# Performance work log

Measured on AMD Instinct MI355X. Metric: run time of the kernel, lower is better.

Reference implementation:

```python
import jax, jax.numpy as jnp
import numpy as np

B, C, T = 8, 64, 128

def _conv(x, w, b, stride=1, pad=1, groups=1):
    y = jax.lax.conv_general_dilated(x, w, (stride, stride), [(pad, pad), (pad, pad)],
                                     feature_group_count=groups,
                                     dimension_numbers=('NCHW', 'OIHW', 'NCHW'))
    return y + b[None, :, None, None]

def _lrelu(x):
    return jnp.where(x > 0, x, 0.1 * x)

def _ps4(A, Bt, Ct, Dt):
    # qiancha(A,B,C,D) interleaves channels with stride 4; PixelShuffle(2) then maps
    # group index j in [0..3] to pixel offset (j//2, j%2): A->(0,0), B->(0,1), C->(1,0), D->(1,1)
    b, c, h, w = A.shape
    s = jnp.stack([A, Bt, Ct, Dt], axis=2).reshape(b, c, 2, 2, h, w)
    return s.transpose(0, 1, 4, 2, 5, 3).reshape(b, c, 2 * h, 2 * w)

def _il2(A, Bt):
    # qiancha2: stride-2 channel interleave
    b, c, h, w = A.shape
    return jnp.stack([A, Bt], axis=2).reshape(b, 2 * c, h, w)

def setup_inputs():
    key = jax.random.key(0)
    ks = jax.random.split(key, 20)
    def w(k, shape):
        return 0.05 * jax.random.normal(k, shape, dtype=jnp.float32)
    d = {}
    d['x'] = jax.random.normal(ks[0], (B, C, T, T), dtype=jnp.float32)
    d['w_hwc'] = w(ks[1], (3 * C, C, 1, 1)); d['b_hwc'] = w(ks[2], (3 * C,))
    d['w_dw'] = w(ks[3], (3 * C, 1, 3, 3)); d['b_dw'] = w(ks[4], (3 * C,))
    d['w_hw'] = w(ks[5], (C, C, 3, 3)); d['b_hw'] = w(ks[6], (C,))
    d['w_cw'] = w(ks[7], (T, T, 3, 3)); d['b_cw'] = w(ks[8], (T,))
    d['w_hc'] = w(ks[9], (T, T, 3, 3)); d['b_hc'] = w(ks[10], (T,))
    d['w_down'] = w(ks[11], (C, 2 * C, 2, 2)); d['b_down'] = w(ks[12], (C,))
    d['w_l1'] = w(ks[13], (C, C, 3, 3)); d['b_l1'] = w(ks[14], (C,))
    d['w_l2'] = w(ks[15], (C, C, 3, 3)); d['b_l2'] = w(ks[16], (C,))
    return d

def reference(x, w_hwc, b_hwc, w_dw, b_dw, w_hw, b_hw, w_cw, b_cw, w_hc, b_hc,
              w_down, b_down, w_l1, b_l1, w_l2, b_l2):
    c = x.shape[1]
    # 1x1 expand then depthwise 3x3 -> three gating maps
    hwc = _conv(_conv(x, w_hwc, b_hwc, pad=0), w_dw, b_dw, pad=1, groups=3 * c)
    HW, CW, HC = jnp.split(hwc, 3, axis=1)
    x_hw = _lrelu(_conv(x, w_hw, b_hw)) * HW
    x_cw = _lrelu(_conv(x.transpose(0, 2, 1, 3), w_cw, b_cw)).transpose(0, 2, 1, 3) * CW
    x_hc = _lrelu(_conv(x.transpose(0, 3, 2, 1), w_hc, b_hc)).transpose(0, 3, 2, 1) * HC
    xqc1 = _ps4(x, x_hw, x_cw, x_hc)
    xqc2 = _ps4(x_hc, x_cw, x_hw, x)
    xqc = _il2(xqc1, xqc2)                              # [B, 2C, 2T, 2T]
    out = _conv(xqc, w_down, b_down, stride=2, pad=0) + x
    out1 = _lrelu(_conv(out, w_l1, b_l1))
    out1 = _lrelu(_conv(out1, w_l2, b_l2))
    return x + out1
```

## Files before the change

kernel.cpp:

```cpp
#include <hip/hip_runtime.h>
#include <hip/hip_bf16.h>

#define BB 8
#define CC 64
#define TT 128
#define PP (TT*TT)
#define C3 192

typedef __hip_bfloat16 bf16;
typedef __attribute__((ext_vector_type(8))) short short8;
typedef __attribute__((ext_vector_type(4))) float floatx4;

__device__ __forceinline__ float b2f(bf16 v){ return __bfloat162float(v); }
__device__ __forceinline__ bf16 f2b(float v){ return __float2bfloat16(v); }
__device__ __forceinline__ short8 lds8(const bf16* p){ return *(const short8*)(const void*)p; }

__global__ void k_wpk(const float* __restrict__ w_down, const float* __restrict__ w_hc,
                      const float* __restrict__ w_cw,  const float* __restrict__ w_hwc,
                      const float* __restrict__ w_hw,  const float* __restrict__ w_l1,
                      const float* __restrict__ w_l2,  const float* __restrict__ w_dw,
                      const float* __restrict__ b_hwc, const float* __restrict__ b_dw,
                      bf16* __restrict__ wpkd,
                      bf16* __restrict__ wpkhw, bf16* __restrict__ wpkl1,
                      bf16* __restrict__ wpkl2, bf16* __restrict__ wpkcw,
                      bf16* __restrict__ wpkhc, bf16* __restrict__ wpkg,
                      float* __restrict__ bg){
  int i = blockIdx.x*256 + threadIdx.x;
  if (i < 147456){
    int j = i & 7, lane = (i>>3) & 63, mm = (i>>9) & 7, kk = (i>>12) & 3, t = i >> 14;
    int m = mm*16 + (lane & 15);
    int k = kk*32 + (lane>>4)*8 + j;
    wpkcw[i] = f2b(w_cw[m*1152 + k*9 + t]);
    wpkhc[i] = f2b(w_hc[m*1152 + k*9 + t]);
  }
  if (i < 36864){
    int j = i & 7, lane = (i>>3) & 63, mm = (i>>9) & 3, kk = (i>>11) & 1, t = i >> 12;
    int oc = mm*16 + (lane & 15);
    int ic = kk*32 + (lane>>4)*8 + j;
    int s = oc*576 + ic*9 + t;
    wpkhw[i] = f2b(w_hw[s]);
    wpkl1[i] = f2b(w_l1[s]);
    wpkl2[i] = f2b(w_l2[s]);
  }
  if (i < 110592){
    int j = i & 7, lane = (i>>3) & 63, rest = i >> 9;
    int mm = rest % 12, tk = rest / 12;
    int oc = mm*16 + (lane & 15);
    int ic = (tk & 1)*32 + (lane>>4)*8 + j;
    int t = tk >> 1;
    wpkg[i] = f2b(w_dw[oc*9 + t] * w_hwc[oc*64 + ic]);
  }
  if (i < 1728){
    int cls = i / C3, oc = i % C3;
    int ch = cls / 3, cw = cls % 3;
    float S = 0.f;
    for (int dh = (ch==0?1:0); dh <= (ch==2?1:2); ++dh)
      for (int dw = (cw==0?1:0); dw <= (cw==2?1:2); ++dw)
        S += w_dw[oc*9 + dh*3 + dw];
    bg[cls*C3 + oc] = b_dw[oc] + b_hwc[oc]*S;
  }
  if (i < 16384){
    int j = i & 7, lane = (i>>3) & 63, mm = (i>>9) & 3, kk = i >> 11;
    int m = mm*16 + (lane & 15);
    int k = kk*32 + (lane>>4)*8 + j;
    int s = k >> 6, c = k & 63;
    wpkd[i] = f2b(w_down[m*512 + c*8 + s] + w_down[m*512 + c*8 + 7 - s]);
  }
}

__global__ void k_pack(const float* __restrict__ x, bf16* __restrict__ xh,
                       bf16* __restrict__ xb16){
  int h = blockIdx.x, b = blockIdx.y;
  __shared__ float xs[64][129];
  for (int idx = threadIdx.x; idx < 2048; idx += 256){
    int c = idx >> 5, w4 = (idx & 31)*4;
    float4 v = *(const float4*)(x + ((size_t)b*CC + c)*PP + h*TT + w4);
    bf16 o4[4] = { f2b(v.x), f2b(v.y), f2b(v.z), f2b(v.w) };
    *(uint2*)(xb16 + ((size_t)b*CC + c)*PP + h*TT + w4) = *(uint2*)o4;
    xs[c][w4] = v.x; xs[c][w4+1] = v.y; xs[c][w4+2] = v.z; xs[c][w4+3] = v.w;
  }
  __syncthreads();
  for (int idx = threadIdx.x; idx < 8192; idx += 256){
    int w = idx >> 6, c = idx & 63;
    xh[(((size_t)b*TT + h)*TT + w)*64 + c] = f2b(xs[c][w]);
  }
}

__global__ void k_xw(const float* __restrict__ x, bf16* __restrict__ xW){
  int c = blockIdx.x, b = blockIdx.y;
  __shared__ float xs2[32][129];
  const float* src = x + ((size_t)b*CC + c)*PP;
  bf16* dst = xW + ((size_t)b*CC + c)*PP;
  for (int s = 0; s < 4; ++s){
    for (int idx = threadIdx.x; idx < 4096; idx += 256){
      int hl = idx >> 7, w = idx & 127;
      xs2[hl][w] = src[(s*32 + hl)*TT + w];
    }
    __syncthreads();
    for (int idx = threadIdx.x; idx < 4096; idx += 256){
      int w = idx >> 5, hl = idx & 31;
      dst[w*TT + s*32 + hl] = f2b(xs2[hl][w]);
    }
    __syncthreads();
  }
}

__global__ __launch_bounds__(256)
void k_g3x3m(const bf16* __restrict__ xh, const bf16* __restrict__ wpkg,
             const float* __restrict__ bg, bf16* __restrict__ g){
  int w0b = blockIdx.x*64, h = blockIdx.y, b = blockIdx.z;
  int tid = threadIdx.x, lane = tid & 63, wv = tid >> 6;
  int nlo = lane & 15, quad = lane >> 4;
  __shared__ bf16 xs[3][66][64];
  for (int idx = tid; idx < 1584; idx += 256){
    int dh = idx / 528, r = idx % 528, wi = r >> 3, ch = r & 7;
    int gh = h + dh - 1, gw = w0b + wi - 1;
    uint4 v = make_uint4(0,0,0,0);
    if (gh >= 0 && gh < TT && gw >= 0 && gw < TT)
      v = *(const uint4*)(xh + (((size_t)b*TT + gh)*TT + gw)*64 + ch*8);
    *(uint4*)(&xs[dh][wi][((ch ^ (wi & 7)))*8]) = v;
  }
  __syncthreads();
  floatx4 acc[3][4] = {};
  #pragma unroll
  for (int t = 0; t < 9; ++t){
    int dh = t/3, dw = t%3;
    int swk = (nlo + dw) & 7;
    #pragma unroll
    for (int kk = 0; kk < 2; ++kk){
      int pc = ((kk*4 + quad) ^ swk)*8;
      short8 bfv[4];
      #pragma unroll
      for (int nn = 0; nn < 4; ++nn)
        bfv[nn] = lds8(&xs[dh][nn*16 + nlo + dw][pc]);
      #pragma unroll
      for (int ml = 0; ml < 3; ++ml){
        short8 a = *(const short8*)(const void*)(wpkg + (((t*2+kk)*12 + wv*3 + ml)*64 + lane)*8);
        #pragma unroll
        for (int nn = 0; nn < 4; ++nn)
          acc[ml][nn] = __builtin_amdgcn_mfma_f32_16x16x32_bf16(a, bfv[nn], acc[ml][nn], 0,0,0);
      }
    }
  }
  int ch_cls3 = ((h == 0) ? 0 : (h == TT-1) ? 2 : 1)*3;
  #pragma unroll
  for (int ml = 0; ml < 3; ++ml){
    int oc0 = (wv*3 + ml)*16 + quad*4;
    #pragma unroll
    for (int nn = 0; nn < 4; ++nn){
      int w = w0b + nn*16 + nlo;
      int cw_cls = (w == 0) ? 0 : (w == TT-1) ? 2 : 1;
      float4 bgv = *(const float4*)(bg + (ch_cls3 + cw_cls)*C3 + oc0);
      int pi = h*TT + w;
      g[((size_t)b*C3 + oc0 + 0)*PP + pi] = f2b(acc[ml][nn][0] + bgv.x);
      g[((size_t)b*C3 + oc0 + 1)*PP + pi] = f2b(acc[ml][nn][1] + bgv.y);
      g[((size_t)b*C3 + oc0 + 2)*PP + pi] = f2b(acc[ml][nn][2] + bgv.z);
      g[((size_t)b*C3 + oc0 + 3)*PP + pi] = f2b(acc[ml][nn][3] + bgv.w);
    }
  }
}

__global__ __launch_bounds__(256)
void k_c3x3m(const bf16* __restrict__ in, const bf16* __restrict__ wpk,
             const float* __restrict__ bias, const bf16* __restrict__ g, int goff,
             const float* __restrict__ resx, bf16* __restrict__ yb,
             float* __restrict__ yf, int mode){
  int h = blockIdx.x, b = blockIdx.y;
  int tid = threadIdx.x, lane = tid & 63, wv = tid >> 6;
  int nlo = lane & 15, quad = lane >> 4;
  __shared__ bf16 xs[3][130][64];
  for (int idx = tid; idx < 3120; idx += 256){
    int dh = idx / 1040, r = idx % 1040, wi = r >> 3, ch = r & 7;
    int gh = h + dh - 1, gw = wi - 1;
    uint4 v = make_uint4(0,0,0,0);
    if (gh >= 0 && gh < TT && gw >= 0 && gw < TT)
      v = *(const uint4*)(in + (((size_t)b*TT + gh)*TT + gw)*64 + ch*8);
    *(uint4*)(&xs[dh][wi][((ch ^ (wi & 7)))*8]) = v;
  }
  __syncthreads();
  floatx4 acc[8] = {};
  #pragma unroll
  for (int t = 0; t < 9; ++t){
    int dh = t/3, dw = t%3;
    int swk = (nlo + dw) & 7;
    #pragma unroll
    for (int kk = 0; kk < 2; ++kk){
      short8 a = *(const short8*)(const void*)(wpk + (((t*2+kk)*4+wv)*64 + lane)*8);
      int pc = ((kk*4 + quad) ^ swk)*8;
      #pragma unroll
      for (int nn = 0; nn < 8; ++nn){
        short8 bf = lds8(&xs[dh][nn*16 + nlo + dw][pc]);
        acc[nn] = __builtin_amdgcn_mfma_f32_16x16x32_bf16(a, bf, acc[nn], 0,0,0);
      }
    }
  }
  int oc0 = wv*16 + quad*4;
  float4 bs = *(const float4*)(bias + oc0);
  float bsa[4] = { bs.x, bs.y, bs.z, bs.w };
  #pragma unroll
  for (int nn = 0; nn < 8; ++nn){
    int w = nn*16 + nlo;
    int pi = h*TT + w;
    if (mode == 0){
      bf16 o4[4];
      #pragma unroll
      for (int r = 0; r < 4; ++r){
        float v = acc[nn][r] + bsa[r];
        v = v > 0.f ? v : 0.1f*v;
        v *= b2f(g[((size_t)b*C3 + goff + oc0 + r)*PP + pi]);
        o4[r] = f2b(v);
      }
      *(uint2*)(yb + ((size_t)b*PP + pi)*64 + oc0) = *(uint2*)o4;
    } else if (mode == 1){
      bf16 o4[4];
      #pragma unroll
      for (int r = 0; r < 4; ++r){
        float v = acc[nn][r] + bsa[r];
        o4[r] = f2b(v > 0.f ? v : 0.1f*v);
      }
      *(uint2*)(yb + ((size_t)b*PP + pi)*64 + oc0) = *(uint2*)o4;
    } else {
      #pragma unroll
      for (int r = 0; r < 4; ++r){
        int oc = oc0 + r;
        float v = acc[nn][r] + bsa[r];
        v = v > 0.f ? v : 0.1f*v;
        yf[((size_t)b*CC + oc)*PP + pi] = v + resx[((size_t)b*CC + oc)*PP + pi];
      }
    }
  }
}

__global__ __launch_bounds__(256)
void k_cwm(const bf16* __restrict__ xW, const bf16* __restrict__ wpkcw,
           const float* __restrict__ bias, const bf16* __restrict__ g,
           bf16* __restrict__ xcw){
  int w0b = blockIdx.x*64, c = blockIdx.y, b = blockIdx.z;
  int tid = threadIdx.x, lane = tid & 63, wv = tid >> 6;
  int nlo = lane & 15, quad = lane >> 4;
  __shared__ bf16 xs[66][128];
  floatx4 acc[2][4] = {};
  for (int dc = 0; dc < 3; ++dc){
    int cc = c + dc - 1;
    if (cc < 0 || cc >= CC) continue;
    __syncthreads();
    for (int idx = tid; idx < 1056; idx += 256){
      int s = idx >> 4, ch = idx & 15;
      int gw = w0b - 1 + s;
      uint4 v = make_uint4(0,0,0,0);
      if (gw >= 0 && gw < TT)
        v = *(const uint4*)(xW + (((size_t)b*CC + cc)*TT + gw)*TT + ch*8);
      *(uint4*)(&xs[s][((ch ^ (s & 7)))*8]) = v;
    }
    __syncthreads();
    #pragma unroll
    for (int dw = 0; dw < 3; ++dw){
      int t = dc*3 + dw;
      int swk = (nlo + dw) & 7;
      #pragma unroll
      for (int kk = 0; kk < 4; ++kk){
        short8 a0 = *(const short8*)(const void*)(wpkcw + (((t*4+kk)*8 + wv*2    )*64 + lane)*8);
        short8 a1 = *(const short8*)(const void*)(wpkcw + (((t*4+kk)*8 + wv*2 + 1)*64 + lane)*8);
        int pc = ((kk*4 + quad) ^ swk)*8;
        #pragma unroll
        for (int nn = 0; nn < 4; ++nn){
          short8 bf = lds8(&xs[nn*16 + nlo + dw][pc]);
          acc[0][nn] = __builtin_amdgcn_mfma_f32_16x16x32_bf16(a0, bf, acc[0][nn], 0,0,0);
          acc[1][nn] = __builtin_amdgcn_mfma_f32_16x16x32_bf16(a1, bf, acc[1][nn], 0,0,0);
        }
      }
    }
  }
  #pragma unroll
  for (int ml = 0; ml < 2; ++ml){
    int ho0 = (wv*2 + ml)*16 + quad*4;
    float4 bs = *(const float4*)(bias + ho0);
    float bsa[4] = { bs.x, bs.y, bs.z, bs.w };
    #pragma unroll
    for (int nn = 0; nn < 4; ++nn){
      int w = w0b + nn*16 + nlo;
      #pragma unroll
      for (int r = 0; r < 4; ++r){
        int ho = ho0 + r;
        float v = acc[ml][nn][r] + bsa[r];
        v = v > 0.f ? v : 0.1f*v;
        v *= b2f(g[((size_t)b*C3 + 64 + c)*PP + ho*TT + w]);
        xcw[((size_t)b*CC + c)*PP + ho*TT + w] = f2b(v);
      }
    }
  }
}

__global__ __launch_bounds__(256)
void k_hcm(const bf16* __restrict__ xb16, const bf16* __restrict__ wpkhc,
           const float* __restrict__ bias, const bf16* __restrict__ g,
           bf16* __restrict__ xhch){
  int h = blockIdx.x, b = blockIdx.y;
  int tid = threadIdx.x, lane = tid & 63, wv = tid >> 6;
  int nlo = lane & 15, quad = lane >> 4;
  __shared__ bf16 xs[66][128];
  floatx4 acc[2][4] = {};
  for (int dh = 0; dh < 3; ++dh){
    int gh = h + dh - 1;
    __syncthreads();
    for (int idx = tid; idx < 1056; idx += 256){
      int s = idx >> 4, ch = idx & 15;
      int cc = s - 1;
      uint4 v = make_uint4(0,0,0,0);
      if (cc >= 0 && cc < CC && gh >= 0 && gh < TT)
        v = *(const uint4*)(xb16 + (((size_t)b*CC + cc)*TT + gh)*TT + ch*8);
      *(uint4*)(&xs[s][((ch ^ (s & 7)))*8]) = v;
    }
    __syncthreads();
    #pragma unroll
    for (int dc = 0; dc < 3; ++dc){
      int t = dh*3 + dc;
      int swk = (nlo + dc) & 7;
      #pragma unroll
      for (int kk = 0; kk < 4; ++kk){
        short8 a0 = *(const short8*)(const void*)(wpkhc + (((t*4+kk)*8 + wv*2    )*64 + lane)*8);
        short8 a1 = *(const short8*)(const void*)(wpkhc + (((t*4+kk)*8 + wv*2 + 1)*64 + lane)*8);
        int pc = ((kk*4 + quad) ^ swk)*8;
        #pragma unroll
        for (int nn = 0; nn < 4; ++nn){
          short8 bf = lds8(&xs[nn*16 + nlo + dc][pc]);
          acc[0][nn] = __builtin_amdgcn_mfma_f32_16x16x32_bf16(a0, bf, acc[0][nn], 0,0,0);
          acc[1][nn] = __builtin_amdgcn_mfma_f32_16x16x32_bf16(a1, bf, acc[1][nn], 0,0,0);
        }
      }
    }
  }
  #pragma unroll
  for (int ml = 0; ml < 2; ++ml){
    int wo0 = (wv*2 + ml)*16 + quad*4;
    float4 bs = *(const float4*)(bias + wo0);
    float bsa[4] = { bs.x, bs.y, bs.z, bs.w };
    #pragma unroll
    for (int nn = 0; nn < 4; ++nn){
      int c = nn*16 + nlo;
      bf16 gg[4];
      *(uint2*)gg = *(const uint2*)(g + ((size_t)b*C3 + 128 + c)*PP + h*TT + wo0);
      #pragma unroll
      for (int r = 0; r < 4; ++r){
        float v = acc[ml][nn][r] + bsa[r];
        v = v > 0.f ? v : 0.1f*v;
        xhch[((size_t)b*PP + h*TT + wo0 + r)*64 + c] = f2b(v * b2f(gg[r]));
      }
    }
  }
}

__global__ __launch_bounds__(256)
void k_downm(const bf16* __restrict__ xh, const bf16* __restrict__ xhwh,
             const bf16* __restrict__ xcwn, const bf16* __restrict__ xhch,
             const bf16* __restrict__ wpkd, const float* __restrict__ x,
             const float* __restrict__ bias, bf16* __restrict__ outh){
  int h = blockIdx.x, b = blockIdx.y;
  int tid = threadIdx.x, lane = tid & 63, wv = tid >> 6;
  int nlo = lane & 15, quad = lane >> 4;
  int p0 = h*TT;
  __shared__ bf16 xs[128][76];
  for (int idx = tid; idx < 1024; idx += 256){
    int c = idx >> 4, w8 = (idx & 15)*8;
    bf16 tmp[8];
    *(uint4*)tmp = *(const uint4*)(xcwn + ((size_t)b*CC + c)*PP + p0 + w8);
    #pragma unroll
    for (int j = 0; j < 8; ++j) xs[w8+j][c] = tmp[j];
  }
  __syncthreads();
  int n0 = wv*32;
  floatx4 acc[4][2] = {};
  #pragma unroll
  for (int kk = 0; kk < 8; ++kk){
    int s = kk >> 1;
    int ko = (kk & 1)*32 + quad*8;
    short8 bfr[2];
    #pragma unroll
    for (int nn = 0; nn < 2; ++nn){
      int p = n0 + nn*16 + nlo;
      if (s == 2){
        bfr[nn] = lds8(&xs[p][ko]);
      } else {
        const bf16* src = (s == 0) ? xh : (s == 1) ? xhwh : xhch;
        bfr[nn] = *(const short8*)(const void*)(src + ((size_t)b*PP + p0 + p)*64 + ko);
      }
    }
    #pragma unroll
    for (int mm = 0; mm < 4; ++mm){
      short8 a = *(const short8*)(const void*)(wpkd + ((kk*4+mm)*64 + lane)*8);
      acc[mm][0] = __builtin_amdgcn_mfma_f32_16x16x32_bf16(a, bfr[0], acc[mm][0], 0,0,0);
      acc[mm][1] = __builtin_amdgcn_mfma_f32_16x16x32_bf16(a, bfr[1], acc[mm][1], 0,0,0);
    }
  }
  #pragma unroll
  for (int mm = 0; mm < 4; ++mm){
    int o0 = mm*16 + quad*4;
    float4 bs = *(const float4*)(bias + o0);
    float bsa[4] = { bs.x, bs.y, bs.z, bs.w };
    #pragma unroll
    for (int nn = 0; nn < 2; ++nn){
      int p = n0 + nn*16 + nlo;
      bf16 o4[4];
      #pragma unroll
      for (int r = 0; r < 4; ++r){
        float v = acc[mm][nn][r] + bsa[r] + x[((size_t)b*CC + o0 + r)*PP + p0 + p];
        o4[r] = f2b(v);
      }
      *(uint2*)(outh + ((size_t)b*PP + p0 + p)*64 + o0) = *(uint2*)o4;
    }
  }
}

extern "C" void kernel_launch(void* const* d_in, const int* in_sizes, int n_in,
                              void* d_out, int out_size, void* d_ws, size_t ws_size,
                              hipStream_t stream) {
  const float* x      = (const float*)d_in[0];
  const float* w_hwc  = (const float*)d_in[1];
  const float* b_hwc  = (const float*)d_in[2];
  const float* w_dw   = (const float*)d_in[3];
  const float* b_dw   = (const float*)d_in[4];
  const float* w_hw   = (const float*)d_in[5];
  const float* b_hw   = (const float*)d_in[6];
  const float* w_cw   = (const float*)d_in[7];
  const float* b_cw   = (const float*)d_in[8];
  const float* w_hc   = (const float*)d_in[9];
  const float* b_hc   = (const float*)d_in[10];
  const float* w_down = (const float*)d_in[11];
  const float* b_down = (const float*)d_in[12];
  const float* w_l1   = (const float*)d_in[13];
  const float* b_l1   = (const float*)d_in[14];
  const float* w_l2   = (const float*)d_in[15];
  const float* b_l2   = (const float*)d_in[16];
  float* out = (float*)d_out;

  char* ws = (char*)d_ws;
  bf16*  wpkd  = (bf16*) (ws + 0);
  float* bg    = (float*)(ws + 36864);
  bf16*  wpkhw = (bf16*) (ws + 65536);
  bf16*  wpkl1 = (bf16*) (ws + 139264);
  bf16*  wpkl2 = (bf16*) (ws + 212992);
  bf16*  wpkcw = (bf16*) (ws + 294912);
  bf16*  wpkhc = (bf16*) (ws + 589824);
  bf16*  wpkg  = (bf16*) (ws + 884736);

  k_wpk<<<576, 256, 0, stream>>>(w_down, w_hc, w_cw, w_hwc, w_hw, w_l1, w_l2,
                                 w_dw, b_hwc, b_dw,
                                 wpkd, wpkhw, wpkl1, wpkl2, wpkcw, wpkhc,
                                 wpkg, bg);

  if (ws_size >= 153092096ull) {
    bf16* g    = (bf16*)(ws + 2097152);
    bf16* xh   = (bf16*)(ws + 52428800);
    bf16* xW   = (bf16*)(ws + 69206016);
    bf16* xb16 = (bf16*)(ws + 85983232);
    bf16* xhwh = (bf16*)(ws + 102760448);
    bf16* xcw  = (bf16*)(ws + 119537664);
    bf16* xhch = (bf16*)(ws + 136314880);
    bf16* outh = xW;
    bf16* o1h  = xb16;

    k_pack<<<dim3(TT, BB), 256, 0, stream>>>(x, xh, xb16);
    k_xw<<<dim3(CC, BB), 256, 0, stream>>>(x, xW);
    k_g3x3m<<<dim3(2, TT, BB), 256, 0, stream>>>(xh, wpkg, bg, g);
    k_c3x3m<<<dim3(TT, BB), 256, 0, stream>>>(xh, wpkhw, b_hw, g, 0, nullptr, xhwh, nullptr, 0);
    k_cwm  <<<dim3(2, CC, BB), 256, 0, stream>>>(xW, wpkcw, b_cw, g, xcw);
    k_hcm  <<<dim3(TT, BB), 256, 0, stream>>>(xb16, wpkhc, b_hc, g, xhch);
    k_downm<<<dim3(TT, BB), 256, 0, stream>>>(xh, xhwh, xcw, xhch, wpkd, x, b_down, outh);
    k_c3x3m<<<dim3(TT, BB), 256, 0, stream>>>(outh, wpkl1, b_l1, nullptr, 0, nullptr, o1h, nullptr, 1);
    k_c3x3m<<<dim3(TT, BB), 256, 0, stream>>>(o1h, wpkl2, b_l2, nullptr, 0, x, nullptr, out, 2);
  } else {
    char* P = ws + 2097152;
    bf16* g_b    = (bf16*)(P);
    bf16* xh_b   = (bf16*)(P + 6291456);
    bf16* xW_b   = (bf16*)(P + 8388608);
    bf16* xb_b   = (bf16*)(P + 10485760);
    bf16* xhwh_b = (bf16*)(P + 12582912);
    bf16* xcw_b  = (bf16*)(P + 14680064);
    bf16* xhch_b = (bf16*)(P + 16777216);
    bf16* outh_b = xW_b;
    bf16* o1h_b  = xb_b;
    for (int b = 0; b < BB; ++b){
      const float* xb = x + (size_t)b*CC*PP;
      float* outb = out + (size_t)b*CC*PP;
      k_pack<<<dim3(TT, 1), 256, 0, stream>>>(xb, xh_b, xb_b);
      k_xw<<<dim3(CC, 1), 256, 0, stream>>>(xb, xW_b);
      k_g3x3m<<<dim3(2, TT, 1), 256, 0, stream>>>(xh_b, wpkg, bg, g_b);
      k_c3x3m<<<dim3(TT, 1), 256, 0, stream>>>(xh_b, wpkhw, b_hw, g_b, 0, nullptr, xhwh_b, nullptr, 0);
      k_cwm  <<<dim3(2, CC, 1), 256, 0, stream>>>(xW_b, wpkcw, b_cw, g_b, xcw_b);
      k_hcm  <<<dim3(TT, 1), 256, 0, stream>>>(xb_b, wpkhc, b_hc, g_b, xhch_b);
      k_downm<<<dim3(TT, 1), 256, 0, stream>>>(xh_b, xhwh_b, xcw_b, xhch_b, wpkd, xb, b_down, outh_b);
      k_c3x3m<<<dim3(TT, 1), 256, 0, stream>>>(outh_b, wpkl1, b_l1, nullptr, 0, nullptr, o1h_b, nullptr, 1);
      k_c3x3m<<<dim3(TT, 1), 256, 0, stream>>>(o1h_b, wpkl2, b_l2, nullptr, 0, xb, nullptr, outb, 2);
    }
  }
}
```

Baseline: 349.8 us.

## Fuse gating-map conv with HW-branch conv sharing one input tile

Merges the gating 3x3 conv kernel and the HW-branch 3x3 conv into a single kernel that loads the input halo tile once and runs both MFMA streams on the same B fragments. The HW gating channels are consumed in registers, so they are never written to or read back from global memory. The remaining gate channels are staged through LDS and written with coalesced 16-byte stores instead of scattered 2-byte stores. It adds register pressure (16 accumulators per thread) and removes one kernel launch and one full re-read of the input.

```diff
diff --git a/kernel.cpp b/kernel.cpp
--- a/kernel.cpp
+++ b/kernel.cpp
@@ -106,8 +106,10 @@
 }
 
 __global__ __launch_bounds__(256)
-void k_g3x3m(const bf16* __restrict__ xh, const bf16* __restrict__ wpkg,
-             const float* __restrict__ bg, bf16* __restrict__ g){
+void k_ghwm(const bf16* __restrict__ xh, const bf16* __restrict__ wpkg,
+            const bf16* __restrict__ wpkhw, const float* __restrict__ bg,
+            const float* __restrict__ b_hw, bf16* __restrict__ xhwh,
+            bf16* __restrict__ g){
   int w0b = blockIdx.x*64, h = blockIdx.y, b = blockIdx.z;
   int tid = threadIdx.x, lane = tid & 63, wv = tid >> 6;
   int nlo = lane & 15, quad = lane >> 4;
@@ -121,7 +123,7 @@
     *(uint4*)(&xs[dh][wi][((ch ^ (wi & 7)))*8]) = v;
   }
   __syncthreads();
-  floatx4 acc[3][4] = {};
+  floatx4 acc[4][4] = {};
   #pragma unroll
   for (int t = 0; t < 9; ++t){
     int dh = t/3, dw = t%3;
@@ -133,36 +135,69 @@
       #pragma unroll
       for (int nn = 0; nn < 4; ++nn)
         bfv[nn] = lds8(&xs[dh][nn*16 + nlo + dw][pc]);
-      #pragma unroll
-      for (int ml = 0; ml < 3; ++ml){
-        short8 a = *(const short8*)(const void*)(wpkg + (((t*2+kk)*12 + wv*3 + ml)*64 + lane)*8);
-        #pragma unroll
-        for (int nn = 0; nn < 4; ++nn)
-          acc[ml][nn] = __builtin_amdgcn_mfma_f32_16x16x32_bf16(a, bfv[nn], acc[ml][nn], 0,0,0);
+      short8 a0 = *(const short8*)(const void*)(wpkhw + (((t*2+kk)*4  + wv   )*64 + lane)*8);
+      short8 a1 = *(const short8*)(const void*)(wpkg  + (((t*2+kk)*12 + wv   )*64 + lane)*8);
+      short8 a2 = *(const short8*)(const void*)(wpkg  + (((t*2+kk)*12 + 4+wv )*64 + lane)*8);
+      short8 a3 = *(const short8*)(const void*)(wpkg  + (((t*2+kk)*12 + 8+wv )*64 + lane)*8);
+      #pragma unroll
+      for (int nn = 0; nn < 4; ++nn){
+        acc[0][nn] = __builtin_amdgcn_mfma_f32_16x16x32_bf16(a0, bfv[nn], acc[0][nn], 0,0,0);
+        acc[1][nn] = __builtin_amdgcn_mfma_f32_16x16x32_bf16(a1, bfv[nn], acc[1][nn], 0,0,0);
+        acc[2][nn] = __builtin_amdgcn_mfma_f32_16x16x32_bf16(a2, bfv[nn], acc[2][nn], 0,0,0);
+        acc[3][nn] = __builtin_amdgcn_mfma_f32_16x16x32_bf16(a3, bfv[nn], acc[3][nn], 0,0,0);
       }
     }
   }
   int ch_cls3 = ((h == 0) ? 0 : (h == TT-1) ? 2 : 1)*3;
-  #pragma unroll
-  for (int ml = 0; ml < 3; ++ml){
-    int oc0 = (wv*3 + ml)*16 + quad*4;
+  int oc0 = wv*16 + quad*4;
+  float4 bhw = *(const float4*)(b_hw + oc0);
+  #pragma unroll
+  for (int nn = 0; nn < 4; ++nn){
+    int w = w0b + nn*16 + nlo;
+    int cw_cls = (w == 0) ? 0 : (w == TT-1) ? 2 : 1;
+    const float* bgrow = bg + (ch_cls3 + cw_cls)*C3;
+    float4 bg0 = *(const float4*)(bgrow + oc0);
+    float bga[4] = { bg0.x, bg0.y, bg0.z, bg0.w };
+    float bha[4] = { bhw.x, bhw.y, bhw.z, bhw.w };
+    bf16 o4[4];
+    #pragma unroll
+    for (int r = 0; r < 4; ++r){
+      float hv = acc[0][nn][r] + bha[r];
+      hv = hv > 0.f ? hv : 0.1f*hv;
+      float gv = b2f(f2b(acc[1][nn][r] + bga[r]));
+      o4[r] = f2b(hv * gv);
+    }
+    *(uint2*)(xhwh + (((size_t)b*PP + h*TT + w))*64 + oc0) = *(uint2*)o4;
+  }
+  __syncthreads();
+  bf16* tb = &xs[0][0][0];
+  #pragma unroll
+  for (int p = 0; p < 2; ++p){
     #pragma unroll
     for (int nn = 0; nn < 4; ++nn){
-      int w = w0b + nn*16 + nlo;
+      int wl = nn*16 + nlo;
+      int w = w0b + wl;
       int cw_cls = (w == 0) ? 0 : (w == TT-1) ? 2 : 1;
-      float4 bgv = *(const float4*)(bg + (ch_cls3 + cw_cls)*C3 + oc0);
-      int pi = h*TT + w;
-      g[((size_t)b*C3 + oc0 + 0)*PP + pi] = f2b(acc[ml][nn][0] + bgv.x);
-      g[((size_t)b*C3 + oc0 + 1)*PP + pi] = f2b(acc[ml][nn][1] + bgv.y);
-      g[((size_t)b*C3 + oc0 + 2)*PP + pi] = f2b(acc[ml][nn][2] + bgv.z);
-      g[((size_t)b*C3 + oc0 + 3)*PP + pi] = f2b(acc[ml][nn][3] + bgv.w);
-    }
+      float4 bgp = *(const float4*)(bg + (ch_cls3 + cw_cls)*C3 + 64 + p*64 + oc0);
+      float bga[4] = { bgp.x, bgp.y, bgp.z, bgp.w };
+      #pragma unroll
+      for (int r = 0; r < 4; ++r)
+        tb[(p*64 + oc0 + r)*72 + wl] = f2b(acc[2+p][nn][r] + bga[r]);
+    }
+  }
+  __syncthreads();
+  #pragma unroll
+  for (int i = 0; i < 4; ++i){
+    int idx = i*256 + tid;
+    int row = idx >> 3, wc = (idx & 7)*8;
+    uint4 v = *(const uint4*)(tb + row*72 + wc);
+    *(uint4*)(g + ((size_t)b*C3 + 64 + row)*PP + h*TT + w0b + wc) = v;
   }
 }
 
 __global__ __launch_bounds__(256)
 void k_c3x3m(const bf16* __restrict__ in, const bf16* __restrict__ wpk,
-             const float* __restrict__ bias, const bf16* __restrict__ g, int goff,
+             const float* __restrict__ bias,
              const float* __restrict__ resx, bf16* __restrict__ yb,
              float* __restrict__ yf, int mode){
   int h = blockIdx.x, b = blockIdx.y;
@@ -201,17 +236,7 @@
   for (int nn = 0; nn < 8; ++nn){
     int w = nn*16 + nlo;
     int pi = h*TT + w;
-    if (mode == 0){
-      bf16 o4[4];
-      #pragma unroll
-      for (int r = 0; r < 4; ++r){
-        float v = acc[nn][r] + bsa[r];
-        v = v > 0.f ? v : 0.1f*v;
-        v *= b2f(g[((size_t)b*C3 + goff + oc0 + r)*PP + pi]);
-        o4[r] = f2b(v);
-      }
-      *(uint2*)(yb + ((size_t)b*PP + pi)*64 + oc0) = *(uint2*)o4;
-    } else if (mode == 1){
+    if (mode == 1){
       bf16 o4[4];
       #pragma unroll
       for (int r = 0; r < 4; ++r){
@@ -461,13 +486,12 @@
 
     k_pack<<<dim3(TT, BB), 256, 0, stream>>>(x, xh, xb16);
     k_xw<<<dim3(CC, BB), 256, 0, stream>>>(x, xW);
-    k_g3x3m<<<dim3(2, TT, BB), 256, 0, stream>>>(xh, wpkg, bg, g);
-    k_c3x3m<<<dim3(TT, BB), 256, 0, stream>>>(xh, wpkhw, b_hw, g, 0, nullptr, xhwh, nullptr, 0);
+    k_ghwm<<<dim3(2, TT, BB), 256, 0, stream>>>(xh, wpkg, wpkhw, bg, b_hw, xhwh, g);
     k_cwm  <<<dim3(2, CC, BB), 256, 0, stream>>>(xW, wpkcw, b_cw, g, xcw);
     k_hcm  <<<dim3(TT, BB), 256, 0, stream>>>(xb16, wpkhc, b_hc, g, xhch);
     k_downm<<<dim3(TT, BB), 256, 0, stream>>>(xh, xhwh, xcw, xhch, wpkd, x, b_down, outh);
-    k_c3x3m<<<dim3(TT, BB), 256, 0, stream>>>(outh, wpkl1, b_l1, nullptr, 0, nullptr, o1h, nullptr, 1);
-    k_c3x3m<<<dim3(TT, BB), 256, 0, stream>>>(o1h, wpkl2, b_l2, nullptr, 0, x, nullptr, out, 2);
+    k_c3x3m<<<dim3(TT, BB), 256, 0, stream>>>(outh, wpkl1, b_l1, nullptr, o1h, nullptr, 1);
+    k_c3x3m<<<dim3(TT, BB), 256, 0, stream>>>(o1h, wpkl2, b_l2, x, nullptr, out, 2);
   } else {
     char* P = ws + 2097152;
     bf16* g_b    = (bf16*)(P);
@@ -484,13 +508,12 @@
       float* outb = out + (size_t)b*CC*PP;
       k_pack<<<dim3(TT, 1), 256, 0, stream>>>(xb, xh_b, xb_b);
       k_xw<<<dim3(CC, 1), 256, 0, stream>>>(xb, xW_b);
-      k_g3x3m<<<dim3(2, TT, 1), 256, 0, stream>>>(xh_b, wpkg, bg, g_b);
-      k_c3x3m<<<dim3(TT, 1), 256, 0, stream>>>(xh_b, wpkhw, b_hw, g_b, 0, nullptr, xhwh_b, nullptr, 0);
+      k_ghwm<<<dim3(2, TT, 1), 256, 0, stream>>>(xh_b, wpkg, wpkhw, bg, b_hw, xhwh_b, g_b);
       k_cwm  <<<dim3(2, CC, 1), 256, 0, stream>>>(xW_b, wpkcw, b_cw, g_b, xcw_b);
       k_hcm  <<<dim3(TT, 1), 256, 0, stream>>>(xb_b, wpkhc, b_hc, g_b, xhch_b);
       k_downm<<<dim3(TT, 1), 256, 0, stream>>>(xh_b, xhwh_b, xcw_b, xhch_b, wpkd, xb, b_down, outh_b);
-      k_c3x3m<<<dim3(TT, 1), 256, 0, stream>>>(outh_b, wpkl1, b_l1, nullptr, 0, nullptr, o1h_b, nullptr, 1);
-      k_c3x3m<<<dim3(TT, 1), 256, 0, stream>>>(o1h_b, wpkl2, b_l2, nullptr, 0, xb, nullptr, outb, 2);
-    }
-  }
-}
+      k_c3x3m<<<dim3(TT, 1), 256, 0, stream>>>(outh_b, wpkl1, b_l1, nullptr, o1h_b, nullptr, 1);
+      k_c3x3m<<<dim3(TT, 1), 256, 0, stream>>>(o1h_b, wpkl2, b_l2, xb, nullptr, outb, 2);
+    }
+  }
+}
```

After: 326.3 us. 6.7% less time.
